# Performance work log

Measured on AMD Instinct MI355X. Metric: run time of the kernel, lower is better.

The kernel has to match this reference:

```python
import jax, jax.numpy as jnp
import numpy as np

NUM_HEADS = 16
D_MODEL = 1024
D_QKV = 64


def _xavier(key, shape):
    # xavier normal over last two dims (fan_in = D_MODEL, fan_out = D_QKV)
    std = float(np.sqrt(2.0 / (shape[-2] + shape[-1])))
    return jax.random.normal(key, shape, dtype=jnp.float32) * std


def setup_inputs() -> dict:
    key = jax.random.key(0)
    ks = jax.random.split(key, 9)
    B, L = 4, 2048
    q = jax.random.normal(ks[0], (B, L, D_MODEL), dtype=jnp.float32)
    k = jax.random.normal(ks[1], (B, L, D_MODEL), dtype=jnp.float32)
    v = jax.random.normal(ks[2], (B, L, D_MODEL), dtype=jnp.float32)
    mask = jax.random.randint(ks[3], (B, L, L), 0, 2, dtype=jnp.int32)
    Wq = _xavier(ks[4], (NUM_HEADS, D_MODEL, D_QKV))
    Wk = _xavier(ks[5], (NUM_HEADS, D_MODEL, D_QKV))
    Wv = _xavier(ks[6], (NUM_HEADS, D_MODEL, D_QKV))
    lim = float(1.0 / np.sqrt(D_MODEL))
    Wo_w = jax.random.uniform(ks[7], (D_MODEL, D_MODEL), minval=-lim, maxval=lim, dtype=jnp.float32)
    Wo_b = jax.random.uniform(ks[8], (D_MODEL,), minval=-lim, maxval=lim, dtype=jnp.float32)
    return {"q": q, "k": k, "v": v, "mask": mask,
            "Wq": Wq, "Wk": Wk, "Wv": Wv, "Wo_w": Wo_w, "Wo_b": Wo_b}


def reference(q, k, v, mask, Wq, Wk, Wv, Wo_w, Wo_b):
    B, L, _ = q.shape
    query = jnp.einsum('blm,nmd->bnld', q, Wq)   # [B,H,L,Dq]
    key_ = jnp.einsum('blm,nmd->bnld', k, Wk)
    value = jnp.einsum('blm,nmd->bnld', v, Wv)
    scores = jnp.einsum('bnld,bnmd->bnlm', query, key_) / jnp.sqrt(
        jnp.asarray(D_QKV, dtype=query.dtype))          # [B,H,L,L]
    scores = jnp.where(mask[:, None, :, :] == 0, jnp.asarray(-1e9, scores.dtype), scores)
    attn = jax.nn.softmax(scores, axis=-1)
    out = jnp.einsum('bnlm,bnmd->bnld', attn, value)     # [B,H,L,Dq]
    out = out.transpose(0, 2, 1, 3).reshape(B, L, D_MODEL)
    return out @ Wo_w.T + Wo_b
```

## Files before the change

kernel.cpp:

```cpp
#include <hip/hip_runtime.h>
#include <stdint.h>

typedef __bf16 bf16;
typedef __bf16 bf16x8 __attribute__((ext_vector_type(8)));
typedef float  f32x4  __attribute__((ext_vector_type(4)));
typedef uint32_t u32;
typedef uint64_t u64;

#define SCALE_L2E 0.18033688011112042f

__device__ __forceinline__ void gld_lds16(const void* gsrc, void* ldst) {
  __builtin_amdgcn_global_load_lds(
      (const __attribute__((address_space(1))) void*)gsrc,
      (__attribute__((address_space(3))) void*)ldst, 16, 0, 0);
}

__global__ void prep(const float* __restrict__ q, const float* __restrict__ k,
                     const float* __restrict__ v, const int* __restrict__ mask,
                     const float* __restrict__ Wq, const float* __restrict__ Wk,
                     const float* __restrict__ Wv, const float* __restrict__ Wo,
                     bf16* __restrict__ qkv, bf16* __restrict__ Wt, u32* __restrict__ mbits) {
  __shared__ float lds[64][65];
  const int z = blockIdx.z;
  const int t = threadIdx.x;
  const int tg = blockIdx.x * 256 + t;
  if (z < 3) {
    const float* in = (z == 0) ? q : (z == 1) ? k : v;
    bf16* o = qkv + (size_t)z * 8388608;
#pragma unroll
    for (int it = 0; it < 2; ++it) {
      int i = tg + it * 524288;
      const float4* p = (const float4*)(in + (size_t)i * 8);
      float4 a = p[0], b = p[1];
      bf16x8 vv;
      vv[0]=(bf16)a.x; vv[1]=(bf16)a.y; vv[2]=(bf16)a.z; vv[3]=(bf16)a.w;
      vv[4]=(bf16)b.x; vv[5]=(bf16)b.y; vv[6]=(bf16)b.z; vv[7]=(bf16)b.w;
      *(bf16x8*)(o + (size_t)i * 8) = vv;
    }
  } else if (z == 3) {
    const int blk = blockIdx.x;
    if (blk < 768) {
      int s = blk >> 8, sub = blk & 255;
      int h = sub >> 4, mblk = sub & 15;
      const float* W = (s == 0) ? Wq : (s == 1) ? Wk : Wv;
      const float* src = W + h * 65536 + mblk * 4096;
#pragma unroll
      for (int i = 0; i < 16; ++i) {
        int idx = t + i * 256;
        lds[idx >> 6][idx & 63] = src[idx];
      }
      __syncthreads();
      int d = t >> 2, o0 = t & 3;
#pragma unroll
      for (int oo = 0; oo < 2; ++oo) {
        int o = o0 + oo * 4;
        bf16x8 vv;
#pragma unroll
        for (int j = 0; j < 8; ++j)
          vv[j] = (bf16)lds[o * 8 + j][d];
        *(bf16x8*)&Wt[(size_t)s * 1048576 + (size_t)(h * 64 + d) * 1024 + mblk * 64 + o * 8] = vv;
      }
    } else if (blk < 832) {
      int idx0 = (blk - 768) * 256 + t;
      for (int i = idx0; i < 131072; i += 16384) {
        const float4* p = (const float4*)&Wo[i * 8];
        float4 a = p[0], b = p[1];
        bf16x8 vv;
        vv[0]=(bf16)a.x; vv[1]=(bf16)a.y; vv[2]=(bf16)a.z; vv[3]=(bf16)a.w;
        vv[4]=(bf16)b.x; vv[5]=(bf16)b.y; vv[6]=(bf16)b.z; vv[7]=(bf16)b.w;
        *(bf16x8*)&Wt[3145728 + (size_t)i * 8] = vv;
      }
    }
  } else {
    for (int idx = tg; idx < 16777216; idx += 524288) {
      int m = mask[idx];
      u64 bal = __ballot(m != 0);
      if ((t & 63) == 0)
        *(u64*)&mbits[idx >> 5] = bal;
    }
  }
}

#define GEMM_CORE(Ap_, Bp_)                                                    \
  __shared__ bf16 sA[2][4096];                                                 \
  __shared__ bf16 sB[2][4096];                                                 \
  const int tid = threadIdx.x;                                                 \
  const int lane = tid & 63, w = tid >> 6;                                     \
  const int c = lane & 15, g = lane >> 4;                                      \
  const int wr = w >> 1, wc = w & 1;                                           \
  const int rr0 = tid >> 3, p0_ = tid & 7;                                     \
  const int l0 = p0_ ^ (rr0 & 7);                                              \
  const size_t so0 = (size_t)(2 * rr0 + (l0 >> 2)) * 1024 + (l0 & 3) * 8;      \
  const int rr1 = (256 + tid) >> 3, p1_ = tid & 7;                             \
  const int l1 = p1_ ^ (rr1 & 7);                                              \
  const size_t so1 = (size_t)(2 * rr1 + (l1 >> 2)) * 1024 + (l1 & 3) * 8;      \
  const bf16* As0 = (Ap_) + so0;                                               \
  const bf16* As1 = (Ap_) + so1;                                               \
  const bf16* Bs0 = (Bp_) + so0;                                               \
  const bf16* Bs1 = (Bp_) + so1;                                               \
  const int fro = (c >> 1) * 128 + ((((c & 1) * 4 + g) ^ (c >> 1)) << 4);      \
  const int abase = wr * 4096 + fro;                                           \
  const int bbase = wc * 4096 + fro;                                           \
  f32x4 acc[4][4] = {};                                                        \
  gld_lds16(As0, (char*)&sA[0][0] + tid * 16);                                 \
  gld_lds16(As1, (char*)&sA[0][0] + 4096 + tid * 16);                          \
  gld_lds16(Bs0, (char*)&sB[0][0] + tid * 16);                                 \
  gld_lds16(Bs1, (char*)&sB[0][0] + 4096 + tid * 16);                          \
  for (int k0 = 0; k0 < 1024; k0 += 32) {                                      \
    __syncthreads();                                                           \
    int cb = (k0 >> 5) & 1, nb = cb ^ 1;                                       \
    if (k0 < 992) {                                                            \
      gld_lds16(As0 + k0 + 32, (char*)&sA[nb][0] + tid * 16);                  \
      gld_lds16(As1 + k0 + 32, (char*)&sA[nb][0] + 4096 + tid * 16);           \
      gld_lds16(Bs0 + k0 + 32, (char*)&sB[nb][0] + tid * 16);                  \
      gld_lds16(Bs1 + k0 + 32, (char*)&sB[nb][0] + 4096 + tid * 16);           \
    }                                                                          \
    const char* a8 = (const char*)&sA[cb][0] + abase;                          \
    const char* b8 = (const char*)&sB[cb][0] + bbase;                          \
    bf16x8 af[4], bfr[4];                                                      \
    _Pragma("unroll")                                                          \
    for (int m = 0; m < 4; ++m)                                                \
      af[m] = *(const bf16x8*)(a8 + m * 1024);                                 \
    _Pragma("unroll")                                                          \
    for (int n = 0; n < 4; ++n)                                                \
      bfr[n] = *(const bf16x8*)(b8 + n * 1024);                                \
    _Pragma("unroll")                                                          \
    for (int m = 0; m < 4; ++m)                                                \
      _Pragma("unroll")                                                        \
      for (int n = 0; n < 4; ++n)                                              \
        acc[m][n] = __builtin_amdgcn_mfma_f32_16x16x32_bf16(af[m], bfr[n], acc[m][n], 0, 0, 0); \
  }

__global__ __launch_bounds__(256, 4)
void proj_fused(const bf16* __restrict__ qkv, const bf16* __restrict__ Wt,
                bf16* __restrict__ Qp, bf16* __restrict__ Kp, bf16* __restrict__ Vt) {
  const int wg = blockIdx.x;
  const bf16* Ap;
  const bf16* Bp;
  int row0, col0, stage;
  if (wg < 1024) {
    int swz = (wg & 7) * 128 + (wg >> 3);
    int bx = swz & 7, by = swz >> 3;
    row0 = by * 128; col0 = bx * 128;
    stage = (row0 >= 8192) ? 1 : 0;
    Ap = qkv + (size_t)row0 * 1024;
    Bp = Wt + (stage ? 1048576 : 0) + (size_t)col0 * 1024;
  } else {
    int w2 = wg - 1024;
    int bz = w2 >> 7, rem = w2 & 127;
    int swz = (rem & 7) * 16 + (rem >> 3);
    int bx = swz & 15, by = swz >> 4;
    row0 = by * 128; col0 = bx * 128;
    stage = 2 + bz;
    Ap = Wt + 2097152 + (size_t)row0 * 1024;
    Bp = qkv + 16777216 + (size_t)bz * 2097152 + (size_t)col0 * 1024;
  }

  GEMM_CORE(Ap, Bp)

  if (stage <= 1) {
    float csc = stage ? 1.0f : SCALE_L2E;
    bf16* dst = stage ? Kp : Qp;
#pragma unroll
    for (int m = 0; m < 4; ++m) {
      int row_base = (row0 & 8191) + wr * 64 + m * 16 + g * 4;
#pragma unroll
      for (int n = 0; n < 4; ++n) {
        int col = col0 + wc * 64 + n * 16 + c;
#pragma unroll
        for (int r = 0; r < 4; ++r) {
          int row = row_base + r;
          int b = row >> 11, l = row & 2047, h = col >> 6, d = col & 63;
          dst[(((size_t)(b * 16 + h) * 2048 + l) << 6) + d] = (bf16)(acc[m][n][r] * csc);
        }
      }
    }
  } else {
    int bz = stage - 2;
#pragma unroll
    for (int m = 0; m < 4; ++m) {
      int row_base = row0 + wr * 64 + m * 16 + g * 4;
#pragma unroll
      for (int n = 0; n < 4; ++n) {
        int col = col0 + wc * 64 + n * 16 + c;
#pragma unroll
        for (int r = 0; r < 4; ++r)
          Vt[((size_t)(bz * 1024 + row_base + r)) * 2048 + col] = (bf16)acc[m][n][r];
      }
    }
  }
}

__global__ __launch_bounds__(256, 4)
void gemm_out(const bf16* __restrict__ X, const bf16* __restrict__ Wot,
              float* __restrict__ out, const float* __restrict__ bias) {
  int lin = blockIdx.y * 8 + blockIdx.x;
  int swz = (lin & 7) * 64 + (lin >> 3);
  int bx = swz & 7, by = swz >> 3;
  const int row0 = by * 128, col0 = bx * 128;
  const bf16* Apx = X + (size_t)row0 * 1024;
  const bf16* Bpx = Wot + (size_t)col0 * 1024;

  GEMM_CORE(Apx, Bpx)

#pragma unroll
  for (int m = 0; m < 4; ++m) {
    int row_base = row0 + wr * 64 + m * 16 + g * 4;
#pragma unroll
    for (int n = 0; n < 4; ++n) {
      int col = col0 + wc * 64 + n * 16 + c;
      float bv = bias[col];
#pragma unroll
      for (int r = 0; r < 4; ++r)
        out[(size_t)(row_base + r) * 1024 + col] = acc[m][n][r] + bv;
    }
  }
}

__global__ __launch_bounds__(256, 4)
void attn_fwd(const bf16* __restrict__ Qp, const bf16* __restrict__ Kp,
              const bf16* __restrict__ Vt, const u32* __restrict__ mbits,
              bf16* __restrict__ X) {
  int lin = blockIdx.y * 16 + blockIdx.x;
  int swz = (lin & 7) * 128 + (lin >> 3);
  int qt = swz & 15, bh = swz >> 4;
  int b = bh >> 4, h = bh & 15;
  int q0 = qt * 128;

  const int tid = threadIdx.x;
  const int lane = tid & 63, w = tid >> 6;
  const int c = lane & 15, g = lane >> 4;

  __shared__ char smem[24704];
  char* sKV = smem;
  char* sPw = smem + 16384 + w * 2048;
  char* sLut = smem + 24576;

  const int c7 = c & 7;
  const int ko0 = c * 128 + ((g ^ c7) << 4);
  const int ko1 = c * 128 + (((4 + g) ^ c7) << 4);
  const int pr_off = (c >> 1) * 128 + ((((c & 1) * 4 + g) ^ (c >> 1)) << 4);
  int pwo[2];
#pragma unroll
  for (int nk = 0; nk < 2; ++nk)
    pwo[nk] = (c >> 1) * 128 + ((((c & 1) * 4 + nk * 2 + (g >> 1)) ^ (c >> 1)) << 4) + (g & 1) * 8;

  const int kr_ = tid >> 3, kb_ = tid & 7;
  const int dK = kr_ * 128 + ((kb_ ^ (kr_ & 7)) << 4);
  const int vd_ = tid >> 2, vk_ = tid & 3;
  const int dV = 4096 + (vd_ >> 1) * 128 + (((((vd_ & 1) << 2) + vk_) ^ ((vd_ >> 1) & 7)) << 4);
  const bf16* gK = Kp + (size_t)bh * 131072 + kr_ * 64 + kb_ * 8;
  const bf16* gV = Vt + ((size_t)(b * 1024 + h * 64 + vd_)) * 2048 + vk_ * 8;

  const bf16* Qbase = Qp + ((size_t)bh * 2048) * 64;
  bf16x8 qf[2][2];
#pragma unroll
  for (int nq = 0; nq < 2; ++nq) {
    int qg = q0 + w * 32 + nq * 16 + c;
#pragma unroll
    for (int kk = 0; kk < 2; ++kk)
      qf[nq][kk] = *(const bf16x8*)&Qbase[(size_t)qg * 64 + kk * 32 + g * 8];
  }

  bf16x8 onesv;
#pragma unroll
  for (int i = 0; i < 8; ++i) onesv[i] = (bf16)1.0f;

  const u32* Mrow0 = mbits + ((size_t)b * 2048 + (q0 + w * 32 + c)) * 64;
  const u32* Mrow1 = mbits + ((size_t)b * 2048 + (q0 + w * 32 + 16 + c)) * 64;
  const int pos0 = 4 * g;
  const int pos1 = 16 + 4 * g;

  f32x4 oacc[4][2] = {};
  f32x4 dacc[2] = {};

  if (tid < 16) {
    u32 n = tid;
    uint2 e;
    e.x = ((n & 1) ? 0xFFFFu : 0u) | ((n & 2) ? 0xFFFF0000u : 0u);
    e.y = ((n & 4) ? 0xFFFFu : 0u) | ((n & 8) ? 0xFFFF0000u : 0u);
    *(uint2*)(sLut + n * 8) = e;
  }
  {
    uint4 kr = *(const uint4*)gK;
    uint4 vr = *(const uint4*)gV;
    *(uint4*)(sKV + dK) = kr;
    *(uint4*)(sKV + dV) = vr;
  }
  u32 mw0 = Mrow0[0], mw1 = Mrow1[0];

  for (int t = 0; t < 64; ++t) {
    __syncthreads();
    const char* kbuf = sKV + ((t & 1) << 13);

    uint2 lm00 = *(const uint2*)(sLut + ((mw0 >> pos0) & 15u) * 8);
    uint2 lm01 = *(const uint2*)(sLut + ((mw0 >> pos1) & 15u) * 8);
    uint2 lm10 = *(const uint2*)(sLut + ((mw1 >> pos0) & 15u) * 8);
    uint2 lm11 = *(const uint2*)(sLut + ((mw1 >> pos1) & 15u) * 8);

    uint4 kr, vr;
    u32 mn0 = 0, mn1 = 0;
    if (t < 63) {
      kr = *(const uint4*)(gK + (size_t)(t + 1) * 2048);
      vr = *(const uint4*)(gV + (size_t)(t + 1) * 32);
      mn0 = Mrow0[t + 1];
      mn1 = Mrow1[t + 1];
    }

    f32x4 st[2][2] = {};
    __builtin_amdgcn_s_setprio(1);
#pragma unroll
    for (int nk = 0; nk < 2; ++nk) {
      bf16x8 kfa = *(const bf16x8*)(kbuf + ko0 + nk * 2048);
      st[nk][0] = __builtin_amdgcn_mfma_f32_16x16x32_bf16(kfa, qf[0][0], st[nk][0], 0, 0, 0);
      st[nk][1] = __builtin_amdgcn_mfma_f32_16x16x32_bf16(kfa, qf[1][0], st[nk][1], 0, 0, 0);
      bf16x8 kfb = *(const bf16x8*)(kbuf + ko1 + nk * 2048);
      st[nk][0] = __builtin_amdgcn_mfma_f32_16x16x32_bf16(kfb, qf[0][1], st[nk][0], 0, 0, 0);
      st[nk][1] = __builtin_amdgcn_mfma_f32_16x16x32_bf16(kfb, qf[1][1], st[nk][1], 0, 0, 0);
    }
    __builtin_amdgcn_s_setprio(0);

#pragma unroll
    for (int nq = 0; nq < 2; ++nq) {
#pragma unroll
      for (int nk = 0; nk < 2; ++nk) {
        float e0 = __builtin_amdgcn_exp2f(st[nk][nq][0]);
        float e1 = __builtin_amdgcn_exp2f(st[nk][nq][1]);
        float e2 = __builtin_amdgcn_exp2f(st[nk][nq][2]);
        float e3 = __builtin_amdgcn_exp2f(st[nk][nq][3]);
        union { bf16 hh[4]; uint2 dd; } pk;
        pk.hh[0] = (bf16)e0; pk.hh[1] = (bf16)e1;
        pk.hh[2] = (bf16)e2; pk.hh[3] = (bf16)e3;
        uint2 lw = nq ? (nk ? lm11 : lm10) : (nk ? lm01 : lm00);
        pk.dd.x &= lw.x;
        pk.dd.y &= lw.y;
        *(uint2*)(sPw + pwo[nk] + nq * 1024) = pk.dd;
      }
    }

    __builtin_amdgcn_s_setprio(1);
    {
      bf16x8 pf0 = *(const bf16x8*)(sPw + pr_off);
      bf16x8 pf1 = *(const bf16x8*)(sPw + pr_off + 1024);
      dacc[0] = __builtin_amdgcn_mfma_f32_16x16x32_bf16(onesv, pf0, dacc[0], 0, 0, 0);
      dacc[1] = __builtin_amdgcn_mfma_f32_16x16x32_bf16(onesv, pf1, dacc[1], 0, 0, 0);
#pragma unroll
      for (int md = 0; md < 4; ++md) {
        bf16x8 vf = *(const bf16x8*)(kbuf + 4096 + pr_off + md * 1024);
        oacc[md][0] = __builtin_amdgcn_mfma_f32_16x16x32_bf16(vf, pf0, oacc[md][0], 0, 0, 0);
        oacc[md][1] = __builtin_amdgcn_mfma_f32_16x16x32_bf16(vf, pf1, oacc[md][1], 0, 0, 0);
      }
    }
    __builtin_amdgcn_s_setprio(0);

    if (t < 63) {
      char* nbuf = sKV + (((t + 1) & 1) << 13);
      *(uint4*)(nbuf + dK) = kr;
      *(uint4*)(nbuf + dV) = vr;
    }
    mw0 = mn0; mw1 = mn1;
  }

  float inv0 = 1.f / dacc[0][0];
  float inv1 = 1.f / dacc[1][0];

  __syncthreads();
  char* Xl = smem;
#pragma unroll
  for (int nq = 0; nq < 2; ++nq) {
    float inv = nq ? inv1 : inv0;
    int ql = w * 32 + nq * 16 + c;
#pragma unroll
    for (int md = 0; md < 4; ++md)
#pragma unroll
      for (int r = 0; r < 4; ++r) {
        int d = md * 16 + g * 4 + r;
        int blk = d >> 3, off = d & 7;
        *(bf16*)(Xl + ql * 128 + ((blk ^ (ql & 7)) << 4) + off * 2) =
            (bf16)(oacc[md][nq][r] * inv);
      }
  }
  __syncthreads();
#pragma unroll
  for (int i = 0; i < 4; ++i) {
    int u = i * 256 + tid;
    int row = u >> 3, blk = u & 7;
    uint4 xv = *(const uint4*)(Xl + row * 128 + ((blk ^ (row & 7)) << 4));
    *(uint4*)&X[(size_t)(b * 2048 + q0 + row) * 1024 + h * 64 + blk * 8] = xv;
  }
}


extern "C" void kernel_launch(void* const* d_in, const int* in_sizes, int n_in,
                              void* d_out, int out_size, void* d_ws, size_t ws_size,
                              hipStream_t stream) {
  const float* q    = (const float*)d_in[0];
  const float* k    = (const float*)d_in[1];
  const float* v    = (const float*)d_in[2];
  const int*   mask = (const int*)d_in[3];
  const float* Wq   = (const float*)d_in[4];
  const float* Wk   = (const float*)d_in[5];
  const float* Wv   = (const float*)d_in[6];
  const float* Wo   = (const float*)d_in[7];
  const float* Wb   = (const float*)d_in[8];

  char* ws = (char*)d_ws;
  bf16* qkv = (bf16*)(ws + 0);
  bf16* Wt  = (bf16*)(ws + 50331648);
  bf16* Qp  = (bf16*)(ws + 58720256);
  bf16* Kp  = (bf16*)(ws + 75497472);
  bf16* Vt  = (bf16*)(ws + 92274688);
  bf16* Xb  = (bf16*)(ws + 109051904);
  u32*  mb  = (u32*) (ws + 125829120);

  prep<<<dim3(2048, 1, 5), 256, 0, stream>>>(q, k, v, mask, Wq, Wk, Wv, Wo, qkv, Wt, mb);

  proj_fused<<<dim3(1536, 1, 1), 256, 0, stream>>>(qkv, Wt, Qp, Kp, Vt);

  attn_fwd<<<dim3(16, 64, 1), 256, 0, stream>>>(Qp, Kp, Vt, mb, Xb);

  gemm_out<<<dim3(8, 64, 1), 256, 0, stream>>>(Xb, Wt + 3145728, (float*)d_out, Wb);
}
```

Measured before the change: 243.3 us.

## Overlap mask bit-packing with projection GEMM and use direct-to-LDS K/V loads

```diff
diff --git a/kernel.cpp b/kernel.cpp
--- a/kernel.cpp
+++ b/kernel.cpp
@@ -16,10 +16,10 @@
 }
 
 __global__ void prep(const float* __restrict__ q, const float* __restrict__ k,
-                     const float* __restrict__ v, const int* __restrict__ mask,
+                     const float* __restrict__ v,
                      const float* __restrict__ Wq, const float* __restrict__ Wk,
                      const float* __restrict__ Wv, const float* __restrict__ Wo,
-                     bf16* __restrict__ qkv, bf16* __restrict__ Wt, u32* __restrict__ mbits) {
+                     bf16* __restrict__ qkv, bf16* __restrict__ Wt) {
   __shared__ float lds[64][65];
   const int z = blockIdx.z;
   const int t = threadIdx.x;
@@ -37,7 +37,7 @@
       vv[4]=(bf16)b.x; vv[5]=(bf16)b.y; vv[6]=(bf16)b.z; vv[7]=(bf16)b.w;
       *(bf16x8*)(o + (size_t)i * 8) = vv;
     }
-  } else if (z == 3) {
+  } else {
     const int blk = blockIdx.x;
     if (blk < 768) {
       int s = blk >> 8, sub = blk & 255;
@@ -70,13 +70,6 @@
         vv[4]=(bf16)b.x; vv[5]=(bf16)b.y; vv[6]=(bf16)b.z; vv[7]=(bf16)b.w;
         *(bf16x8*)&Wt[3145728 + (size_t)i * 8] = vv;
       }
-    }
-  } else {
-    for (int idx = tg; idx < 16777216; idx += 524288) {
-      int m = mask[idx];
-      u64 bal = __ballot(m != 0);
-      if ((t & 63) == 0)
-        *(u64*)&mbits[idx >> 5] = bal;
     }
   }
 }
@@ -133,20 +126,32 @@
 
 __global__ __launch_bounds__(256, 4)
 void proj_fused(const bf16* __restrict__ qkv, const bf16* __restrict__ Wt,
-                bf16* __restrict__ Qp, bf16* __restrict__ Kp, bf16* __restrict__ Vt) {
+                bf16* __restrict__ Qp, bf16* __restrict__ Kp, bf16* __restrict__ Vt,
+                const int* __restrict__ mask, u32* __restrict__ mbits) {
   const int wg = blockIdx.x;
+  if (wg % 3 == 2) {
+    int tg = (wg / 3) * 256 + threadIdx.x;
+    for (int idx = tg; idx < 16777216; idx += 196608) {
+      int m = mask[idx];
+      u64 bal = __ballot(m != 0);
+      if ((threadIdx.x & 63) == 0)
+        *(u64*)&mbits[idx >> 5] = bal;
+    }
+    return;
+  }
+  const int cw = (wg / 3) * 2 + (wg % 3);
   const bf16* Ap;
   const bf16* Bp;
   int row0, col0, stage;
-  if (wg < 1024) {
-    int swz = (wg & 7) * 128 + (wg >> 3);
+  if (cw < 1024) {
+    int swz = (cw & 7) * 128 + (cw >> 3);
     int bx = swz & 7, by = swz >> 3;
     row0 = by * 128; col0 = bx * 128;
     stage = (row0 >= 8192) ? 1 : 0;
     Ap = qkv + (size_t)row0 * 1024;
     Bp = Wt + (stage ? 1048576 : 0) + (size_t)col0 * 1024;
   } else {
-    int w2 = wg - 1024;
+    int w2 = cw - 1024;
     int bz = w2 >> 7, rem = w2 & 127;
     int swz = (rem & 7) * 16 + (rem >> 3);
     int bx = swz & 15, by = swz >> 4;
@@ -245,12 +250,13 @@
   for (int nk = 0; nk < 2; ++nk)
     pwo[nk] = (c >> 1) * 128 + ((((c & 1) * 4 + nk * 2 + (g >> 1)) ^ (c >> 1)) << 4) + (g & 1) * 8;
 
-  const int kr_ = tid >> 3, kb_ = tid & 7;
-  const int dK = kr_ * 128 + ((kb_ ^ (kr_ & 7)) << 4);
-  const int vd_ = tid >> 2, vk_ = tid & 3;
-  const int dV = 4096 + (vd_ >> 1) * 128 + (((((vd_ & 1) << 2) + vk_) ^ ((vd_ >> 1) & 7)) << 4);
-  const bf16* gK = Kp + (size_t)bh * 131072 + kr_ * 64 + kb_ * 8;
-  const bf16* gV = Vt + ((size_t)(b * 1024 + h * 64 + vd_)) * 2048 + vk_ * 8;
+  const int ksr = tid >> 3;
+  const int ksl = (tid & 7) ^ (ksr & 7);
+  const bf16* gK = Kp + (size_t)bh * 131072 + ksr * 64 + ksl * 8;
+  const int vrr = tid >> 3;
+  const int vl = (tid & 7) ^ (vrr & 7);
+  const int vd = 2 * vrr + (vl >> 2), vko = vl & 3;
+  const bf16* gV = Vt + ((size_t)(b * 1024 + h * 64 + vd)) * 2048 + vko * 8;
 
   const bf16* Qbase = Qp + ((size_t)bh * 2048) * 64;
   bf16x8 qf[2][2];
@@ -281,28 +287,27 @@
     e.y = ((n & 4) ? 0xFFFFu : 0u) | ((n & 8) ? 0xFFFF0000u : 0u);
     *(uint2*)(sLut + n * 8) = e;
   }
-  {
-    uint4 kr = *(const uint4*)gK;
-    uint4 vr = *(const uint4*)gV;
-    *(uint4*)(sKV + dK) = kr;
-    *(uint4*)(sKV + dV) = vr;
-  }
+  gld_lds16(gK, sKV + tid * 16);
+  gld_lds16(gV, sKV + 4096 + tid * 16);
   u32 mw0 = Mrow0[0], mw1 = Mrow1[0];
 
   for (int t = 0; t < 64; ++t) {
     __syncthreads();
     const char* kbuf = sKV + ((t & 1) << 13);
+
+    if (t < 63) {
+      char* nbuf = sKV + (((t + 1) & 1) << 13);
+      gld_lds16(gK + (size_t)(t + 1) * 2048, nbuf + tid * 16);
+      gld_lds16(gV + (size_t)(t + 1) * 32, nbuf + 4096 + tid * 16);
+    }
 
     uint2 lm00 = *(const uint2*)(sLut + ((mw0 >> pos0) & 15u) * 8);
     uint2 lm01 = *(const uint2*)(sLut + ((mw0 >> pos1) & 15u) * 8);
     uint2 lm10 = *(const uint2*)(sLut + ((mw1 >> pos0) & 15u) * 8);
     uint2 lm11 = *(const uint2*)(sLut + ((mw1 >> pos1) & 15u) * 8);
 
-    uint4 kr, vr;
     u32 mn0 = 0, mn1 = 0;
     if (t < 63) {
-      kr = *(const uint4*)(gK + (size_t)(t + 1) * 2048);
-      vr = *(const uint4*)(gV + (size_t)(t + 1) * 32);
       mn0 = Mrow0[t + 1];
       mn1 = Mrow1[t + 1];
     }
@@ -353,11 +358,6 @@
     }
     __builtin_amdgcn_s_setprio(0);
 
-    if (t < 63) {
-      char* nbuf = sKV + (((t + 1) & 1) << 13);
-      *(uint4*)(nbuf + dK) = kr;
-      *(uint4*)(nbuf + dV) = vr;
-    }
     mw0 = mn0; mw1 = mn1;
   }
 
@@ -413,9 +413,9 @@
   bf16* Xb  = (bf16*)(ws + 109051904);
   u32*  mb  = (u32*) (ws + 125829120);
 
-  prep<<<dim3(2048, 1, 5), 256, 0, stream>>>(q, k, v, mask, Wq, Wk, Wv, Wo, qkv, Wt, mb);
-
-  proj_fused<<<dim3(1536, 1, 1), 256, 0, stream>>>(qkv, Wt, Qp, Kp, Vt);
+  prep<<<dim3(2048, 1, 4), 256, 0, stream>>>(q, k, v, Wq, Wk, Wv, Wo, qkv, Wt);
+
+  proj_fused<<<dim3(2304, 1, 1), 256, 0, stream>>>(qkv, Wt, Qp, Kp, Vt, mask, mb);
 
   attn_fwd<<<dim3(16, 64, 1), 256, 0, stream>>>(Qp, Kp, Vt, mb, Xb);
 
```

Measured after the change: 285.6 us. 17.4% more time.
